# Optimization experiments

Measured on AMD Instinct MI355X. Metric: run time of the kernel, lower is better.

Reference implementation:

```python
import jax, jax.numpy as jnp
import numpy as np

IN_NC = 7


def setup_inputs() -> dict:
    key = jax.random.key(0)
    ks = jax.random.split(key, 32)
    B, H, W = 4, 192, 192
    Cf, O, L = 64, 64, 32  # in_fea, out_fea, len=max(64//16,32)
    d = {}
    d['fea'] = jax.random.normal(ks[0], (B, Cf, H, W), jnp.float32)
    d['inputs'] = jax.random.normal(ks[1], (B, IN_NC, H, W), jnp.float32)
    j = 2
    for i in range(3):
        k = 2 * i + 1
        oc = IN_NC * 3 * k * k
        d['dw_w%d' % i] = jax.random.normal(ks[j], (Cf, 1, k, k), jnp.float32) * 0.05; j += 1
        d['dw_b%d' % i] = jnp.zeros((Cf,), jnp.float32)
        d['pw_w%d' % i] = jax.random.normal(ks[j], (oc, Cf), jnp.float32) * 0.05; j += 1
        d['pw_b%d' % i] = jnp.zeros((oc,), jnp.float32)
        d['dcn_w%d' % i] = jax.random.normal(ks[j], (O, IN_NC, k, k), jnp.float32) * 0.05; j += 1
        d['dcn_b%d' % i] = jnp.zeros((O,), jnp.float32)
    d['attn_w'] = jax.random.normal(ks[j], (O, 3 * O), jnp.float32) * 0.05; j += 1
    d['attn_b'] = jnp.zeros((O,), jnp.float32)
    d['fc_w'] = jax.random.normal(ks[j], (L, O), jnp.float32) * 0.05; j += 1
    d['fc_b'] = jnp.zeros((L,), jnp.float32)
    for i in range(3):
        d['fcs_w%d' % i] = jax.random.normal(ks[j], (O, L), jnp.float32) * 0.05; j += 1
        d['fcs_b%d' % i] = jnp.zeros((O,), jnp.float32)
    d['conv_w'] = jax.random.normal(ks[j], (O, 3 * O), jnp.float32) * 0.05; j += 1
    d['conv_b'] = jnp.zeros((O,), jnp.float32)
    return d


def _dw_conv(x, w, b):
    # depthwise conv, stride 1, SAME padding (pad = k//2 for odd k)
    y = jax.lax.conv_general_dilated(x, w, window_strides=(1, 1), padding='SAME',
                                     dimension_numbers=('NCHW', 'OIHW', 'NCHW'),
                                     feature_group_count=x.shape[1])
    return y + b[None, :, None, None]


def _pw_conv(x, w, b):
    return jnp.einsum('bchw,oc->bohw', x, w) + b[None, :, None, None]


def _mdcn(x, offset, mask, w, b, k):
    # Modulated deformable conv, deformable_groups == C (one channel per group),
    # stride 1, padding k//2. offset: [B, C*2*K, H, W] as (c, k, (dy,dx)); mask: [B, C*K, H, W].
    B, C, H, W = x.shape
    K = k * k
    pad = k // 2
    off = offset.reshape(B, C, K, 2, H, W)
    m = mask.reshape(B, C, K, H, W)
    ky = (jnp.arange(K) // k).astype(jnp.float32)
    kx = (jnp.arange(K) % k).astype(jnp.float32)
    py = off[:, :, :, 0] + (ky[:, None, None] + jnp.arange(H, dtype=jnp.float32)[None, :, None] - pad)
    px = off[:, :, :, 1] + (kx[:, None, None] + jnp.arange(W, dtype=jnp.float32)[None, None, :] - pad)
    y0 = jnp.floor(py)
    x0 = jnp.floor(px)
    wy = py - y0
    wx = px - x0
    bi = jnp.arange(B)[:, None, None, None, None]
    ci = jnp.arange(C)[None, :, None, None, None]

    def gather(yi, xi):
        valid = (yi >= 0) & (yi < H) & (xi >= 0) & (xi < W)
        yc = jnp.clip(yi, 0, H - 1).astype(jnp.int32)
        xc = jnp.clip(xi, 0, W - 1).astype(jnp.int32)
        return jnp.where(valid, x[bi, ci, yc, xc], 0.0)

    v00 = gather(y0, x0)
    v01 = gather(y0, x0 + 1)
    v10 = gather(y0 + 1, x0)
    v11 = gather(y0 + 1, x0 + 1)
    samp = (v00 * (1 - wy) * (1 - wx) + v01 * (1 - wy) * wx
            + v10 * wy * (1 - wx) + v11 * wy * wx) * m  # [B,C,K,H,W]
    O = w.shape[0]
    return jnp.einsum('bckhw,ock->bohw', samp, w.reshape(O, C, K)) + b[None, :, None, None]


def reference(fea, inputs,
              dw_w0, dw_b0, pw_w0, pw_b0, dcn_w0, dcn_b0,
              dw_w1, dw_b1, pw_w1, pw_b1, dcn_w1, dcn_b1,
              dw_w2, dw_b2, pw_w2, pw_b2, dcn_w2, dcn_b2,
              attn_w, attn_b, fc_w, fc_b,
              fcs_w0, fcs_b0, fcs_w1, fcs_b1, fcs_w2, fcs_b2,
              conv_w, conv_b):
    dw_w = [dw_w0, dw_w1, dw_w2]; dw_b = [dw_b0, dw_b1, dw_b2]
    pw_w = [pw_w0, pw_w1, pw_w2]; pw_b = [pw_b0, pw_b1, pw_b2]
    dcn_w = [dcn_w0, dcn_w1, dcn_w2]; dcn_b = [dcn_b0, dcn_b1, dcn_b2]
    fcs_w = [fcs_w0, fcs_w1, fcs_w2]; fcs_b = [fcs_b0, fcs_b1, fcs_b2]
    outs = []
    for i in range(3):
        k = 2 * i + 1
        ds = k * k
        om = _pw_conv(_dw_conv(fea, dw_w[i], dw_b[i]), pw_w[i], pw_b[i])
        offset = om[:, :IN_NC * 2 * ds]
        mask = jax.nn.sigmoid(om[:, IN_NC * 2 * ds:])
        outs.append(jax.nn.relu(_mdcn(inputs, offset, mask, dcn_w[i], dcn_b[i], k)))
    out = jnp.stack(outs, axis=1)  # [B, 3, O, H, W]
    B, T, C, H, W = out.shape
    att = jax.nn.relu(_pw_conv(out.reshape(B, T * C, H, W), attn_w, attn_b))
    att = jnp.mean(att, axis=(2, 3), keepdims=True)  # GAP -> [B, O, 1, 1]
    att = jax.nn.relu(_pw_conv(att, fc_w, fc_b))      # [B, L, 1, 1]
    atts = jnp.stack([_pw_conv(att, fcs_w[i], fcs_b[i]) for i in range(3)], axis=1)  # [B,3,O,1,1]
    out = out * atts
    out = jax.nn.relu(_pw_conv(out.reshape(B, T * C, H, W), conv_w, conv_b))
    return out
```

## Files before the change

### kernel.cpp

```cpp
#include <hip/hip_runtime.h>
#include <math.h>

#define HH 192
#define WW 192
#define HWP (192*192)
#define BB 4
#define CF 64
#define NC 7
#define OO 64
#define NTOT (BB*HWP)
#define PIX_BLOCKS (HWP/256)

typedef float f32x16 __attribute__((ext_vector_type(16)));
typedef float f32x4  __attribute__((ext_vector_type(4)));

template<int k>
__global__ __launch_bounds__(256)
void dwv_kernel(const float* __restrict__ fea, const float* __restrict__ w,
                const float* __restrict__ bias, float* __restrict__ out) {
    constexpr int pad = k / 2;
    int idx = blockIdx.x * 256 + threadIdx.x;
    int xq = idx % 48;
    int x0 = xq * 4;
    int hpos = (idx / 48) % HH;
    int plane = idx / (48 * HH);
    int c = plane % CF;
    const float* f = fea + (size_t)plane * HWP;

    float wk[k * k];
#pragma unroll
    for (int i = 0; i < k * k; ++i) wk[i] = w[c * k * k + i];

    float acc0 = 0.f, acc1 = 0.f, acc2 = 0.f, acc3 = 0.f;
#pragma unroll
    for (int dy = 0; dy < k; ++dy) {
        int y = hpos + dy - pad;
        if (y < 0 || y >= HH) continue;
        const float* row = f + y * WW;
        float4 q0 = (x0 >= 4) ? *(const float4*)(row + x0 - 4) : make_float4(0.f, 0.f, 0.f, 0.f);
        float4 q1 = *(const float4*)(row + x0);
        float4 q2 = (x0 + 4 < WW) ? *(const float4*)(row + x0 + 4) : make_float4(0.f, 0.f, 0.f, 0.f);
        float wnd[8] = {q0.z, q0.w, q1.x, q1.y, q1.z, q1.w, q2.x, q2.y};
#pragma unroll
        for (int dx = 0; dx < k; ++dx) {
            float wt = wk[dy * k + dx];
            acc0 += wnd[0 + dx + 2 - pad] * wt;
            acc1 += wnd[1 + dx + 2 - pad] * wt;
            acc2 += wnd[2 + dx + 2 - pad] * wt;
            acc3 += wnd[3 + dx + 2 - pad] * wt;
        }
    }
    float b = bias[c];
    float4 o = make_float4(acc0 + b, acc1 + b, acc2 + b, acc3 + b);
    *(float4*)(out + (size_t)plane * HWP + hpos * WW + x0) = o;
}

__global__ void transpose_kernel(const float* __restrict__ in, float* __restrict__ out,
                                 int rows, int cols) {
    int idx = blockIdx.x * 256 + threadIdx.x;
    if (idx >= rows * cols) return;
    int r = idx / cols, c = idx % cols;
    out[c * rows + r] = in[idx];
}

__global__ __launch_bounds__(256)
void pw_gemm_kernel(const float* __restrict__ pw_w, const float* __restrict__ pw_b,
                    const float* __restrict__ dw, float* __restrict__ om,
                    int src0, int n_yx, int src1, int M) {
    __shared__ float As[64][68];
    __shared__ float Bs[64][132];
    const int ntiles = NTOT / 128;
    int ntile = blockIdx.x % ntiles;
    int mtile = blockIdx.x / ntiles;
    int nb0 = ntile * 128;
    int mb0 = mtile * 64;
    int tid = threadIdx.x;

    {
        int m = tid & 63;
        int kq = tid >> 6;
        int gm = mb0 + m;
        int srow = (gm < M) ? ((gm < n_yx) ? (src0 + gm) : (src1 + (gm - n_yx))) : src0;
        const float* ap = pw_w + (size_t)srow * CF;
#pragma unroll
        for (int i = 0; i < 4; ++i) {
            int k0 = (kq * 4 + i) * 4;
            float4 v = *(const float4*)(ap + k0);
            As[k0 + 0][m] = v.x; As[k0 + 1][m] = v.y;
            As[k0 + 2][m] = v.z; As[k0 + 3][m] = v.w;
        }
    }
    {
        int b = nb0 / HWP;
        int p0 = nb0 % HWP;
        const float* bp = dw + (size_t)b * CF * HWP + p0;
#pragma unroll
        for (int i = 0; i < 8; ++i) {
            int idx = tid + i * 256;
            int kk = idx >> 5;
            int f4 = idx & 31;
            float4 v = *(const float4*)(bp + (size_t)kk * HWP + f4 * 4);
            *(float4*)&Bs[kk][f4 * 4] = v;
        }
    }
    __syncthreads();

    int tm = (tid & 15) * 4;
    int tn = (tid >> 4) * 8;
    f32x4 aA0 = 0.f, aA1 = 0.f, aB0 = 0.f, aB1 = 0.f;
    f32x4 aC0 = 0.f, aC1 = 0.f, aD0 = 0.f, aD1 = 0.f;
#pragma unroll 8
    for (int kk = 0; kk < 64; ++kk) {
        f32x4 a  = *(const f32x4*)&As[kk][tm];
        f32x4 b0 = *(const f32x4*)&Bs[kk][tn];
        f32x4 b1 = *(const f32x4*)&Bs[kk][tn + 4];
#pragma unroll
        for (int j = 0; j < 4; ++j) {
            aA0[j] += a[0] * b0[j];  aA1[j] += a[0] * b1[j];
            aB0[j] += a[1] * b0[j];  aB1[j] += a[1] * b1[j];
            aC0[j] += a[2] * b0[j];  aC1[j] += a[2] * b1[j];
            aD0[j] += a[3] * b0[j];  aD1[j] += a[3] * b1[j];
        }
    }
    {
        int gm = mb0 + tm;
        float* dst = om + (size_t)gm * NTOT + nb0 + tn;
        if (gm < M) {
            float bi = pw_b[(gm < n_yx) ? (src0 + gm) : (src1 + gm - n_yx)];
#pragma unroll
            for (int j = 0; j < 4; ++j) { dst[j] = aA0[j] + bi; dst[4 + j] = aA1[j] + bi; }
        }
        gm++; dst += NTOT;
        if (gm < M) {
            float bi = pw_b[(gm < n_yx) ? (src0 + gm) : (src1 + gm - n_yx)];
#pragma unroll
            for (int j = 0; j < 4; ++j) { dst[j] = aB0[j] + bi; dst[4 + j] = aB1[j] + bi; }
        }
        gm++; dst += NTOT;
        if (gm < M) {
            float bi = pw_b[(gm < n_yx) ? (src0 + gm) : (src1 + gm - n_yx)];
#pragma unroll
            for (int j = 0; j < 4; ++j) { dst[j] = aC0[j] + bi; dst[4 + j] = aC1[j] + bi; }
        }
        gm++; dst += NTOT;
        if (gm < M) {
            float bi = pw_b[(gm < n_yx) ? (src0 + gm) : (src1 + gm - n_yx)];
#pragma unroll
            for (int j = 0; j < 4; ++j) { dst[j] = aD0[j] + bi; dst[4 + j] = aD1[j] + bi; }
        }
    }
}

template<int k>
__global__ __launch_bounds__(256)
void sample_kernel(const float* __restrict__ om, const float* __restrict__ inputs,
                   float* __restrict__ sbuf, int t0, int t1) {
    constexpr int K = k * k;
    constexpr int pad = k / 2;
    const int T = t1 - t0;
    int g = blockIdx.x / (NTOT / 256);
    int nb = blockIdx.x % (NTOT / 256);
    int n = nb * 256 + threadIdx.x;
    int b = n / HWP, p = n % HWP;
    int h = p / WW, wq = p % WW;
    const float* inb = inputs + (size_t)b * NC * HWP;
    int half = (T + 1) >> 1;
    int i0 = g * half;
    int i1 = min(T, i0 + half);
#pragma unroll 2
    for (int i = i0; i < i1; ++i) {
        int r = t0 + i;
        float oy = om[(size_t)(2 * i) * NTOT + n];
        float ox = om[(size_t)(2 * i + 1) * NTOT + n];
        float mr = om[(size_t)(2 * T + i) * NTOT + n];
        int c = r / K;
        int kk = r - c * K;
        int ky = kk / k, kx = kk - ky * k;
        const float* inc_ = inb + (size_t)c * HWP;
        float m = 1.f / (1.f + __expf(-mr));
        float py = oy + (float)(ky + h - pad);
        float px = ox + (float)(kx + wq - pad);
        float y0 = floorf(py), x0 = floorf(px);
        float wyf = py - y0, wxf = px - x0;
        int iy0 = (int)y0, ix0 = (int)x0;
        bool y0v = (iy0 >= 0) && (iy0 < HH);
        bool y1v = (iy0 + 1 >= 0) && (iy0 + 1 < HH);
        bool x0v = (ix0 >= 0) && (ix0 < WW);
        bool x1v = (ix0 + 1 >= 0) && (ix0 + 1 < WW);
        int yc0 = min(max(iy0, 0), HH - 1), yc1 = min(max(iy0 + 1, 0), HH - 1);
        int xc0 = min(max(ix0, 0), WW - 1), xc1 = min(max(ix0 + 1, 0), WW - 1);
        float v00 = 0.f, v01 = 0.f, v10 = 0.f, v11 = 0.f;
        if (y0v) {
            if (x0v) v00 = inc_[yc0 * WW + xc0];
            if (x1v) v01 = inc_[yc0 * WW + xc1];
        }
        if (y1v) {
            if (x0v) v10 = inc_[yc1 * WW + xc0];
            if (x1v) v11 = inc_[yc1 * WW + xc1];
        }
        float s = (v00 * (1.f - wyf) * (1.f - wxf) + v01 * (1.f - wyf) * wxf +
                   v10 * wyf * (1.f - wxf) + v11 * wyf * wxf) * m;
        sbuf[(size_t)i * NTOT + n] = s;
    }
}

__global__ __launch_bounds__(256)
void acc_gemm_kernel(const float* __restrict__ wt,
                     const float* __restrict__ bias,
                     const float* __restrict__ sbuf,
                     float* __restrict__ outbuf, int t_slot,
                     int t0, int t1, int flags) {
    __shared__ float As[64][68];
    __shared__ float Bs[64][132];
    const int T = t1 - t0;
    int nb0 = blockIdx.x * 128;
    int tid = threadIdx.x;

    for (int i4 = tid; i4 < T * 16; i4 += 256) {
        int row = i4 >> 4, c4 = (i4 & 15) * 4;
        float4 v = *(const float4*)(wt + (size_t)(t0 + row) * OO + c4);
        As[row][c4] = v.x; As[row][c4 + 1] = v.y; As[row][c4 + 2] = v.z; As[row][c4 + 3] = v.w;
    }
    for (int i4 = tid; i4 < T * 32; i4 += 256) {
        int row = i4 >> 5, f4 = (i4 & 31) * 4;
        float4 v = *(const float4*)(sbuf + (size_t)row * NTOT + nb0 + f4);
        *(float4*)&Bs[row][f4] = v;
    }
    __syncthreads();

    int tm = (tid & 15) * 4;
    int tn = (tid >> 4) * 8;
    f32x4 aA0 = 0.f, aA1 = 0.f, aB0 = 0.f, aB1 = 0.f;
    f32x4 aC0 = 0.f, aC1 = 0.f, aD0 = 0.f, aD1 = 0.f;
#pragma unroll 2
    for (int kk = 0; kk < T; ++kk) {
        f32x4 a  = *(const f32x4*)&As[kk][tm];
        f32x4 b0 = *(const f32x4*)&Bs[kk][tn];
        f32x4 b1 = *(const f32x4*)&Bs[kk][tn + 4];
#pragma unroll
        for (int j = 0; j < 4; ++j) {
            aA0[j] += a[0] * b0[j];  aA1[j] += a[0] * b1[j];
            aB0[j] += a[1] * b0[j];  aB1[j] += a[1] * b1[j];
            aC0[j] += a[2] * b0[j];  aC1[j] += a[2] * b1[j];
            aD0[j] += a[3] * b0[j];  aD1[j] += a[3] * b1[j];
        }
    }

    int b = nb0 / HWP, p0 = nb0 % HWP;
    f32x4 accs[8] = {aA0, aA1, aB0, aB1, aC0, aC1, aD0, aD1};
#pragma unroll
    for (int row = 0; row < 4; ++row) {
        int ch = tm + row;
        float* ptr = outbuf + ((size_t)((b * 3 + t_slot) * OO + ch)) * HWP + p0 + tn;
        f32x4 lo = accs[row * 2], hi = accs[row * 2 + 1];
        if (!(flags & 1)) {
            f32x4 o0 = *(const f32x4*)ptr;
            f32x4 o1 = *(const f32x4*)(ptr + 4);
#pragma unroll
            for (int j = 0; j < 4; ++j) { lo[j] += o0[j]; hi[j] += o1[j]; }
        }
        if (flags & 2) {
            float bi = bias[ch];
#pragma unroll
            for (int j = 0; j < 4; ++j) {
                lo[j] += bi; hi[j] += bi;
                lo[j] = lo[j] > 0.f ? lo[j] : 0.f;
                hi[j] = hi[j] > 0.f ? hi[j] : 0.f;
            }
        }
        *(f32x4*)ptr = lo;
        *(f32x4*)(ptr + 4) = hi;
    }
}

__global__ __launch_bounds__(256)
void branch_k1_kernel(const float* __restrict__ fea,
                      const float* __restrict__ dw_w0, const float* __restrict__ dw_b0,
                      const float* __restrict__ pw_w, const float* __restrict__ pw_b,
                      const float* __restrict__ inputs,
                      const float* __restrict__ dcn_wt, const float* __restrict__ dcn_b,
                      float* __restrict__ outbuf) {
    __shared__ float lw[21 * 64];
    for (int i = threadIdx.x; i < 21 * 16; i += 256)
        ((float4*)lw)[i] = ((const float4*)pw_w)[i];
    __syncthreads();
    int gid = blockIdx.x;
    int b = gid / PIX_BLOCKS;
    int p = (gid % PIX_BLOCKS) * 256 + threadIdx.x;
    int h = p / WW, wq = p % WW;
    const float* inb = inputs + (size_t)b * NC * HWP;

    f32x16 dwv0, dwv1, dwv2, dwv3;
    {
        const float* fp = fea + (size_t)(b * CF) * HWP + p;
#pragma unroll
        for (int j = 0; j < 16; ++j) dwv0[j] = fp[(size_t)j * HWP] * dw_w0[j] + dw_b0[j];
#pragma unroll
        for (int j = 0; j < 16; ++j) dwv1[j] = fp[(size_t)(16 + j) * HWP] * dw_w0[16 + j] + dw_b0[16 + j];
#pragma unroll
        for (int j = 0; j < 16; ++j) dwv2[j] = fp[(size_t)(32 + j) * HWP] * dw_w0[32 + j] + dw_b0[32 + j];
#pragma unroll
        for (int j = 0; j < 16; ++j) dwv3[j] = fp[(size_t)(48 + j) * HWP] * dw_w0[48 + j] + dw_b0[48 + j];
    }
    f32x16 acc0, acc1, acc2, acc3;
#pragma unroll
    for (int j = 0; j < 16; ++j) { acc0[j] = 0.f; acc1[j] = 0.f; acc2[j] = 0.f; acc3[j] = 0.f; }

    for (int r = 0; r < NC; ++r) {
        const float* wy = lw + (2 * r) * 64;
        const float* wx = wy + 64;
        const float* wm = lw + (14 + r) * 64;
        const float* inc_ = inb + (size_t)r * HWP;
        float oy = pw_b[2 * r], ox = pw_b[2 * r + 1], om = pw_b[14 + r];
#pragma unroll
        for (int j = 0; j < 16; ++j) { oy += wy[j] * dwv0[j];      ox += wx[j] * dwv0[j];      om += wm[j] * dwv0[j]; }
#pragma unroll
        for (int j = 0; j < 16; ++j) { oy += wy[16 + j] * dwv1[j]; ox += wx[16 + j] * dwv1[j]; om += wm[16 + j] * dwv1[j]; }
#pragma unroll
        for (int j = 0; j < 16; ++j) { oy += wy[32 + j] * dwv2[j]; ox += wx[32 + j] * dwv2[j]; om += wm[32 + j] * dwv2[j]; }
#pragma unroll
        for (int j = 0; j < 16; ++j) { oy += wy[48 + j] * dwv3[j]; ox += wx[48 + j] * dwv3[j]; om += wm[48 + j] * dwv3[j]; }
        float m = 1.f / (1.f + __expf(-om));
        float py = oy + (float)h;
        float px = ox + (float)wq;
        float y0 = floorf(py), x0 = floorf(px);
        float wyf = py - y0, wxf = px - x0;
        int iy0 = (int)y0, ix0 = (int)x0;
        bool y0v = (iy0 >= 0) && (iy0 < HH);
        bool y1v = (iy0 + 1 >= 0) && (iy0 + 1 < HH);
        bool x0v = (ix0 >= 0) && (ix0 < WW);
        bool x1v = (ix0 + 1 >= 0) && (ix0 + 1 < WW);
        int yc0 = min(max(iy0, 0), HH - 1), yc1 = min(max(iy0 + 1, 0), HH - 1);
        int xc0 = min(max(ix0, 0), WW - 1), xc1 = min(max(ix0 + 1, 0), WW - 1);
        float v00 = 0.f, v01 = 0.f, v10 = 0.f, v11 = 0.f;
        if (y0v) {
            if (x0v) v00 = inc_[yc0 * WW + xc0];
            if (x1v) v01 = inc_[yc0 * WW + xc1];
        }
        if (y1v) {
            if (x0v) v10 = inc_[yc1 * WW + xc0];
            if (x1v) v11 = inc_[yc1 * WW + xc1];
        }
        float s = (v00 * (1.f - wyf) * (1.f - wxf) + v01 * (1.f - wyf) * wxf +
                   v10 * wyf * (1.f - wxf) + v11 * wyf * wxf) * m;
        const float* dt = dcn_wt + (size_t)r * OO;
#pragma unroll
        for (int j = 0; j < 16; ++j) acc0[j] += s * dt[j];
#pragma unroll
        for (int j = 0; j < 16; ++j) acc1[j] += s * dt[16 + j];
#pragma unroll
        for (int j = 0; j < 16; ++j) acc2[j] += s * dt[32 + j];
#pragma unroll
        for (int j = 0; j < 16; ++j) acc3[j] += s * dt[48 + j];
    }
    float* op = outbuf + (size_t)(b * 3 * OO) * HWP + p;
#pragma unroll
    for (int j = 0; j < 16; ++j) { float v = acc0[j] + dcn_b[j];      op[(size_t)j * HWP] = v > 0.f ? v : 0.f; }
#pragma unroll
    for (int j = 0; j < 16; ++j) { float v = acc1[j] + dcn_b[16 + j]; op[(size_t)(16 + j) * HWP] = v > 0.f ? v : 0.f; }
#pragma unroll
    for (int j = 0; j < 16; ++j) { float v = acc2[j] + dcn_b[32 + j]; op[(size_t)(32 + j) * HWP] = v > 0.f ? v : 0.f; }
#pragma unroll
    for (int j = 0; j < 16; ++j) { float v = acc3[j] + dcn_b[48 + j]; op[(size_t)(48 + j) * HWP] = v > 0.f ? v : 0.f; }
}

__global__ __launch_bounds__(256)
void attn_sum_kernel(const float* __restrict__ outbuf, const float* __restrict__ attn_wt,
                     const float* __restrict__ attn_b, float* __restrict__ partial) {
    int g = blockIdx.x & 1;
    int blk = blockIdx.x >> 1;
    int b = blk / PIX_BLOCKS;
    int pb = blk % PIX_BLOCKS;
    int p = pb * 256 + threadIdx.x;
    const float* ob = outbuf + (size_t)(b * 192) * HWP + p;
    f32x16 a0, a1;
#pragma unroll
    for (int j = 0; j < 16; ++j) { a0[j] = attn_b[g * 32 + j]; a1[j] = attn_b[g * 32 + 16 + j]; }
    for (int c = 0; c < 192; ++c) {
        float v = ob[(size_t)c * HWP];
        const float* wt = attn_wt + c * OO + g * 32;
#pragma unroll
        for (int j = 0; j < 16; ++j) a0[j] += v * wt[j];
#pragma unroll
        for (int j = 0; j < 16; ++j) a1[j] += v * wt[16 + j];
    }
    __shared__ float red[4][32];
    int lane = threadIdx.x & 63, wv = threadIdx.x >> 6;
#pragma unroll
    for (int o = 0; o < 32; ++o) {
        float v = (o < 16) ? a0[o] : a1[o - 16];
        v = v > 0.f ? v : 0.f;
        v += __shfl_down(v, 32);
        v += __shfl_down(v, 16);
        v += __shfl_down(v, 8);
        v += __shfl_down(v, 4);
        v += __shfl_down(v, 2);
        v += __shfl_down(v, 1);
        if (lane == 0) red[wv][o] = v;
    }
    __syncthreads();
    if (threadIdx.x < 32) {
        int o = threadIdx.x;
        partial[((size_t)(b * PIX_BLOCKS + pb) * 2 + g) * 32 + o] =
            red[0][o] + red[1][o] + red[2][o] + red[3][o];
    }
}

__global__ void attn_finish_kernel(const float* __restrict__ partial,
                                   const float* __restrict__ fc_w, const float* __restrict__ fc_b,
                                   const float* __restrict__ fcs_w0, const float* __restrict__ fcs_b0,
                                   const float* __restrict__ fcs_w1, const float* __restrict__ fcs_b1,
                                   const float* __restrict__ fcs_w2, const float* __restrict__ fcs_b2,
                                   float* __restrict__ atts) {
    int b = blockIdx.x;
    __shared__ float attm[OO];
    __shared__ float fcv[32];
    int tid = threadIdx.x;
    if (tid < OO) {
        int g = tid >> 5, o = tid & 31;
        float s = 0.f;
        for (int blk = 0; blk < PIX_BLOCKS; ++blk)
            s += partial[((size_t)(b * PIX_BLOCKS + blk) * 2 + g) * 32 + o];
        attm[tid] = s / (float)HWP;
    }
    __syncthreads();
    if (tid < 32) {
        float s = fc_b[tid];
        for (int o = 0; o < OO; ++o) s += fc_w[tid * OO + o] * attm[o];
        fcv[tid] = s > 0.f ? s : 0.f;
    }
    __syncthreads();
    if (tid < OO) {
        {
            float s = fcs_b0[tid];
            for (int j = 0; j < 32; ++j) s += fcs_w0[tid * 32 + j] * fcv[j];
            atts[b * 192 + 0 * OO + tid] = s;
        }
        {
            float s = fcs_b1[tid];
            for (int j = 0; j < 32; ++j) s += fcs_w1[tid * 32 + j] * fcv[j];
            atts[b * 192 + 1 * OO + tid] = s;
        }
        {
            float s = fcs_b2[tid];
            for (int j = 0; j < 32; ++j) s += fcs_w2[tid * 32 + j] * fcv[j];
            atts[b * 192 + 2 * OO + tid] = s;
        }
    }
}

__global__ __launch_bounds__(256)
void final_kernel(const float* __restrict__ outbuf, const float* __restrict__ atts,
                  const float* __restrict__ conv_wt, const float* __restrict__ conv_b,
                  float* __restrict__ out) {
    int g = blockIdx.x & 1;
    int blk = blockIdx.x >> 1;
    int b = blk / PIX_BLOCKS;
    int p = (blk % PIX_BLOCKS) * 256 + threadIdx.x;
    const float* ob = outbuf + (size_t)(b * 192) * HWP + p;
    const float* at = atts + b * 192;
    f32x16 a0, a1;
#pragma unroll
    for (int j = 0; j < 16; ++j) { a0[j] = conv_b[g * 32 + j]; a1[j] = conv_b[g * 32 + 16 + j]; }
    for (int c = 0; c < 192; ++c) {
        float v = ob[(size_t)c * HWP] * at[c];
        const float* wt = conv_wt + c * OO + g * 32;
#pragma unroll
        for (int j = 0; j < 16; ++j) a0[j] += v * wt[j];
#pragma unroll
        for (int j = 0; j < 16; ++j) a1[j] += v * wt[16 + j];
    }
    float* op = out + ((size_t)(b * OO) + g * 32) * HWP + p;
#pragma unroll
    for (int j = 0; j < 16; ++j) op[(size_t)j * HWP] = a0[j] > 0.f ? a0[j] : 0.f;
#pragma unroll
    for (int j = 0; j < 16; ++j) op[(size_t)(16 + j) * HWP] = a1[j] > 0.f ? a1[j] : 0.f;
}

extern "C" void kernel_launch(void* const* d_in, const int* in_sizes, int n_in,
                              void* d_out, int out_size, void* d_ws, size_t ws_size,
                              hipStream_t stream) {
    const float* fea    = (const float*)d_in[0];
    const float* inputs = (const float*)d_in[1];
    const float* dw_w[3]  = {(const float*)d_in[2],  (const float*)d_in[8],  (const float*)d_in[14]};
    const float* dw_b[3]  = {(const float*)d_in[3],  (const float*)d_in[9],  (const float*)d_in[15]};
    const float* pw_w[3]  = {(const float*)d_in[4],  (const float*)d_in[10], (const float*)d_in[16]};
    const float* pw_b[3]  = {(const float*)d_in[5],  (const float*)d_in[11], (const float*)d_in[17]};
    const float* dcn_w[3] = {(const float*)d_in[6],  (const float*)d_in[12], (const float*)d_in[18]};
    const float* dcn_b[3] = {(const float*)d_in[7],  (const float*)d_in[13], (const float*)d_in[19]};
    const float* attn_w = (const float*)d_in[20];
    const float* attn_b = (const float*)d_in[21];
    const float* fc_w   = (const float*)d_in[22];
    const float* fc_b   = (const float*)d_in[23];
    const float* fcs_w[3] = {(const float*)d_in[24], (const float*)d_in[26], (const float*)d_in[28]};
    const float* fcs_b[3] = {(const float*)d_in[25], (const float*)d_in[27], (const float*)d_in[29]};
    const float* conv_w = (const float*)d_in[30];
    const float* conv_b = (const float*)d_in[31];
    float* out = (float*)d_out;

    const size_t F_OUTBUF = (size_t)BB * 3 * OO * HWP;
    const size_t F_SMALL  = 36864 + 768 + 512 + 4096 + 11264 + 12288 + 12288;
    float* W = (float*)d_ws;
    float* outbuf = W;            W += F_OUTBUF;
    size_t avail = (ws_size / 4 > F_OUTBUF + F_SMALL) ? (ws_size / 4 - F_OUTBUF - F_SMALL) : 0;
    int T = (int)(avail / (4 * (size_t)NTOT));
    if (T > 64) T = 64;
    if (T < 1) T = 1;
    float* om = W;                W += (size_t)3 * T * NTOT;
    float* sbuf = W;              W += (size_t)T * NTOT;
    float* partial = W;           W += 36864;
    float* atts = W;              W += 768;
    float* dcn_wt0 = W;           W += 512;
    float* dcn_wt1 = W;           W += 4096;
    float* dcn_wt2 = W;           W += 11264;
    float* attn_wt = W;           W += 12288;
    float* conv_wt = W;           W += 12288;
    float* dwscr = out;

    transpose_kernel<<<(192 * 64 + 255) / 256, 256, 0, stream>>>(attn_w, attn_wt, 64, 192);
    transpose_kernel<<<(192 * 64 + 255) / 256, 256, 0, stream>>>(conv_w, conv_wt, 64, 192);
    transpose_kernel<<<(7 * 64 + 255) / 256, 256, 0, stream>>>(dcn_w[0], dcn_wt0, 64, 7);
    transpose_kernel<<<(63 * 64 + 255) / 256, 256, 0, stream>>>(dcn_w[1], dcn_wt1, 64, 63);
    transpose_kernel<<<(175 * 64 + 255) / 256, 256, 0, stream>>>(dcn_w[2], dcn_wt2, 64, 175);

    const int dwv_grid = (BB * CF * HH * 48) / 256;
    const int pix_grid = BB * PIX_BLOCKS;
    const int samp_grid = 2 * (NTOT / 256);
    const int acc_grid = NTOT / 128;
    const int ntiles = NTOT / 128;

    dwv_kernel<5><<<dwv_grid, 256, 0, stream>>>(fea, dw_w[2], dw_b[2], dwscr);
    {
        const int TT = 175;
        for (int t0 = 0; t0 < TT; t0 += T) {
            int t1 = (t0 + T < TT) ? (t0 + T) : TT;
            int Tc = t1 - t0, M = 3 * Tc;
            int mt = (M + 63) / 64;
            pw_gemm_kernel<<<mt * ntiles, 256, 0, stream>>>(pw_w[2], pw_b[2], dwscr, om,
                                                            2 * t0, 2 * Tc, 2 * TT + t0, M);
            sample_kernel<5><<<samp_grid, 256, 0, stream>>>(om, inputs, sbuf, t0, t1);
            int flags = (t0 == 0 ? 1 : 0) | (t1 == TT ? 2 : 0);
            acc_gemm_kernel<<<acc_grid, 256, 0, stream>>>(dcn_wt2, dcn_b[2], sbuf, outbuf,
                                                          2, t0, t1, flags);
        }
    }
    dwv_kernel<3><<<dwv_grid, 256, 0, stream>>>(fea, dw_w[1], dw_b[1], dwscr);
    {
        const int TT = 63;
        for (int t0 = 0; t0 < TT; t0 += T) {
            int t1 = (t0 + T < TT) ? (t0 + T) : TT;
            int Tc = t1 - t0, M = 3 * Tc;
            int mt = (M + 63) / 64;
            pw_gemm_kernel<<<mt * ntiles, 256, 0, stream>>>(pw_w[1], pw_b[1], dwscr, om,
                                                            2 * t0, 2 * Tc, 2 * TT + t0, M);
            sample_kernel<3><<<samp_grid, 256, 0, stream>>>(om, inputs, sbuf, t0, t1);
            int flags = (t0 == 0 ? 1 : 0) | (t1 == TT ? 2 : 0);
            acc_gemm_kernel<<<acc_grid, 256, 0, stream>>>(dcn_wt1, dcn_b[1], sbuf, outbuf,
                                                          1, t0, t1, flags);
        }
    }
    branch_k1_kernel<<<pix_grid, 256, 0, stream>>>(fea, dw_w[0], dw_b[0], pw_w[0], pw_b[0],
                                                   inputs, dcn_wt0, dcn_b[0], outbuf);

    attn_sum_kernel<<<2 * pix_grid, 256, 0, stream>>>(outbuf, attn_wt, attn_b, partial);
    attn_finish_kernel<<<BB, 64, 0, stream>>>(partial, fc_w, fc_b,
                                              fcs_w[0], fcs_b[0], fcs_w[1], fcs_b[1],
                                              fcs_w[2], fcs_b[2], atts);
    final_kernel<<<2 * pix_grid, 256, 0, stream>>>(outbuf, atts, conv_wt, conv_b, out);
}
```

Baseline: 741.3 us.

## Rewrite attention and final 1x1 convs as LDS-tiled register-blocked GEMMs

Replaces the per-pixel attention-sum and final 1x1-conv kernels with shared-memory tiled GEMM kernels. Each block covers 64 output channels by 128 pixels and loads weight and activation tiles into LDS in 64-channel chunks. Each thread computes a 4x8 register tile. The attention kernel reduces ReLU outputs across pixel groups in LDS and writes 64-wide partial sums, so the partial buffer is doubled. The aim is to stop reading outbuf twice (once per output-channel half) and to cut the scalar weight loads in the inner loop, at the cost of more LDS use and barriers.

```diff
diff --git a/kernel.cpp b/kernel.cpp
--- a/kernel.cpp
+++ b/kernel.cpp
@@ -10,6 +10,7 @@
 #define OO 64
 #define NTOT (BB*HWP)
 #define PIX_BLOCKS (HWP/256)
+#define PBLK2 (HWP/128)
 
 typedef float f32x16 __attribute__((ext_vector_type(16)));
 typedef float f32x4  __attribute__((ext_vector_type(4)));
@@ -365,44 +366,73 @@
 }
 
 __global__ __launch_bounds__(256)
-void attn_sum_kernel(const float* __restrict__ outbuf, const float* __restrict__ attn_wt,
-                     const float* __restrict__ attn_b, float* __restrict__ partial) {
-    int g = blockIdx.x & 1;
-    int blk = blockIdx.x >> 1;
-    int b = blk / PIX_BLOCKS;
-    int pb = blk % PIX_BLOCKS;
-    int p = pb * 256 + threadIdx.x;
-    const float* ob = outbuf + (size_t)(b * 192) * HWP + p;
-    f32x16 a0, a1;
-#pragma unroll
-    for (int j = 0; j < 16; ++j) { a0[j] = attn_b[g * 32 + j]; a1[j] = attn_b[g * 32 + 16 + j]; }
-    for (int c = 0; c < 192; ++c) {
-        float v = ob[(size_t)c * HWP];
-        const float* wt = attn_wt + c * OO + g * 32;
-#pragma unroll
-        for (int j = 0; j < 16; ++j) a0[j] += v * wt[j];
-#pragma unroll
-        for (int j = 0; j < 16; ++j) a1[j] += v * wt[16 + j];
-    }
-    __shared__ float red[4][32];
-    int lane = threadIdx.x & 63, wv = threadIdx.x >> 6;
-#pragma unroll
-    for (int o = 0; o < 32; ++o) {
-        float v = (o < 16) ? a0[o] : a1[o - 16];
-        v = v > 0.f ? v : 0.f;
-        v += __shfl_down(v, 32);
-        v += __shfl_down(v, 16);
-        v += __shfl_down(v, 8);
-        v += __shfl_down(v, 4);
-        v += __shfl_down(v, 2);
-        v += __shfl_down(v, 1);
-        if (lane == 0) red[wv][o] = v;
-    }
+void attn_gemm_kernel(const float* __restrict__ outbuf, const float* __restrict__ attn_wt,
+                      const float* __restrict__ attn_b, float* __restrict__ partial) {
+    __shared__ float As[64][68];
+    __shared__ float Bs[64][132];
+    __shared__ float red[16][68];
+    int nb0 = blockIdx.x * 128;
+    int b = nb0 / HWP, p0 = nb0 % HWP;
+    int tid = threadIdx.x;
+    int tm = (tid & 15) * 4;
+    int tn = (tid >> 4) * 8;
+
+    f32x4 aA0 = 0.f, aA1 = 0.f, aB0 = 0.f, aB1 = 0.f;
+    f32x4 aC0 = 0.f, aC1 = 0.f, aD0 = 0.f, aD1 = 0.f;
+    for (int kc = 0; kc < 3; ++kc) {
+        for (int i4 = tid; i4 < 64 * 16; i4 += 256) {
+            int row = i4 >> 4, c4 = (i4 & 15) * 4;
+            float4 v = *(const float4*)(attn_wt + (size_t)(kc * 64 + row) * OO + c4);
+            As[row][c4] = v.x; As[row][c4 + 1] = v.y; As[row][c4 + 2] = v.z; As[row][c4 + 3] = v.w;
+        }
+        const float* bp = outbuf + ((size_t)(b * 192 + kc * 64)) * HWP + p0;
+        for (int i4 = tid; i4 < 64 * 32; i4 += 256) {
+            int row = i4 >> 5, f4 = (i4 & 31) * 4;
+            float4 v = *(const float4*)(bp + (size_t)row * HWP + f4);
+            *(float4*)&Bs[row][f4] = v;
+        }
+        __syncthreads();
+#pragma unroll 4
+        for (int kk = 0; kk < 64; ++kk) {
+            f32x4 a  = *(const f32x4*)&As[kk][tm];
+            f32x4 b0 = *(const f32x4*)&Bs[kk][tn];
+            f32x4 b1 = *(const f32x4*)&Bs[kk][tn + 4];
+#pragma unroll
+            for (int j = 0; j < 4; ++j) {
+                aA0[j] += a[0] * b0[j];  aA1[j] += a[0] * b1[j];
+                aB0[j] += a[1] * b0[j];  aB1[j] += a[1] * b1[j];
+                aC0[j] += a[2] * b0[j];  aC1[j] += a[2] * b1[j];
+                aD0[j] += a[3] * b0[j];  aD1[j] += a[3] * b1[j];
+            }
+        }
+        __syncthreads();
+    }
+    float bsum[4];
+    {
+        f32x4 accs[8] = {aA0, aA1, aB0, aB1, aC0, aC1, aD0, aD1};
+#pragma unroll
+        for (int row = 0; row < 4; ++row) {
+            float bi = attn_b[tm + row];
+            float s = 0.f;
+#pragma unroll
+            for (int j = 0; j < 4; ++j) {
+                float v0 = accs[row * 2][j] + bi;
+                float v1 = accs[row * 2 + 1][j] + bi;
+                s += (v0 > 0.f ? v0 : 0.f) + (v1 > 0.f ? v1 : 0.f);
+            }
+            bsum[row] = s;
+        }
+    }
+    int pg = tid >> 4;
+#pragma unroll
+    for (int row = 0; row < 4; ++row) red[pg][tm + row] = bsum[row];
     __syncthreads();
-    if (threadIdx.x < 32) {
-        int o = threadIdx.x;
-        partial[((size_t)(b * PIX_BLOCKS + pb) * 2 + g) * 32 + o] =
-            red[0][o] + red[1][o] + red[2][o] + red[3][o];
+    if (tid < 64) {
+        float s = 0.f;
+#pragma unroll
+        for (int g = 0; g < 16; ++g) s += red[g][tid];
+        int lb = p0 / 128;
+        partial[((size_t)(b * PBLK2 + lb)) * OO + tid] = s;
     }
 }
 
@@ -417,10 +447,9 @@
     __shared__ float fcv[32];
     int tid = threadIdx.x;
     if (tid < OO) {
-        int g = tid >> 5, o = tid & 31;
         float s = 0.f;
-        for (int blk = 0; blk < PIX_BLOCKS; ++blk)
-            s += partial[((size_t)(b * PIX_BLOCKS + blk) * 2 + g) * 32 + o];
+        for (int blk = 0; blk < PBLK2; ++blk)
+            s += partial[((size_t)(b * PBLK2 + blk)) * OO + tid];
         attm[tid] = s / (float)HWP;
     }
     __syncthreads();
@@ -450,31 +479,66 @@
 }
 
 __global__ __launch_bounds__(256)
-void final_kernel(const float* __restrict__ outbuf, const float* __restrict__ atts,
-                  const float* __restrict__ conv_wt, const float* __restrict__ conv_b,
-                  float* __restrict__ out) {
-    int g = blockIdx.x & 1;
-    int blk = blockIdx.x >> 1;
-    int b = blk / PIX_BLOCKS;
-    int p = (blk % PIX_BLOCKS) * 256 + threadIdx.x;
-    const float* ob = outbuf + (size_t)(b * 192) * HWP + p;
+void final_gemm_kernel(const float* __restrict__ outbuf, const float* __restrict__ atts,
+                       const float* __restrict__ conv_wt, const float* __restrict__ conv_b,
+                       float* __restrict__ out) {
+    __shared__ float As[64][68];
+    __shared__ float Bs[64][132];
+    int nb0 = blockIdx.x * 128;
+    int b = nb0 / HWP, p0 = nb0 % HWP;
+    int tid = threadIdx.x;
+    int tm = (tid & 15) * 4;
+    int tn = (tid >> 4) * 8;
     const float* at = atts + b * 192;
-    f32x16 a0, a1;
-#pragma unroll
-    for (int j = 0; j < 16; ++j) { a0[j] = conv_b[g * 32 + j]; a1[j] = conv_b[g * 32 + 16 + j]; }
-    for (int c = 0; c < 192; ++c) {
-        float v = ob[(size_t)c * HWP] * at[c];
-        const float* wt = conv_wt + c * OO + g * 32;
-#pragma unroll
-        for (int j = 0; j < 16; ++j) a0[j] += v * wt[j];
-#pragma unroll
-        for (int j = 0; j < 16; ++j) a1[j] += v * wt[16 + j];
-    }
-    float* op = out + ((size_t)(b * OO) + g * 32) * HWP + p;
-#pragma unroll
-    for (int j = 0; j < 16; ++j) op[(size_t)j * HWP] = a0[j] > 0.f ? a0[j] : 0.f;
-#pragma unroll
-    for (int j = 0; j < 16; ++j) op[(size_t)(16 + j) * HWP] = a1[j] > 0.f ? a1[j] : 0.f;
+
+    f32x4 aA0 = 0.f, aA1 = 0.f, aB0 = 0.f, aB1 = 0.f;
+    f32x4 aC0 = 0.f, aC1 = 0.f, aD0 = 0.f, aD1 = 0.f;
+    for (int kc = 0; kc < 3; ++kc) {
+        for (int i4 = tid; i4 < 64 * 16; i4 += 256) {
+            int row = i4 >> 4, c4 = (i4 & 15) * 4;
+            float4 v = *(const float4*)(conv_wt + (size_t)(kc * 64 + row) * OO + c4);
+            As[row][c4] = v.x; As[row][c4 + 1] = v.y; As[row][c4 + 2] = v.z; As[row][c4 + 3] = v.w;
+        }
+        const float* bp = outbuf + ((size_t)(b * 192 + kc * 64)) * HWP + p0;
+        for (int i4 = tid; i4 < 64 * 32; i4 += 256) {
+            int row = i4 >> 5, f4 = (i4 & 31) * 4;
+            float sc = at[kc * 64 + row];
+            float4 v = *(const float4*)(bp + (size_t)row * HWP + f4);
+            Bs[row][f4] = v.x * sc; Bs[row][f4 + 1] = v.y * sc;
+            Bs[row][f4 + 2] = v.z * sc; Bs[row][f4 + 3] = v.w * sc;
+        }
+        __syncthreads();
+#pragma unroll 4
+        for (int kk = 0; kk < 64; ++kk) {
+            f32x4 a  = *(const f32x4*)&As[kk][tm];
+            f32x4 b0 = *(const f32x4*)&Bs[kk][tn];
+            f32x4 b1 = *(const f32x4*)&Bs[kk][tn + 4];
+#pragma unroll
+            for (int j = 0; j < 4; ++j) {
+                aA0[j] += a[0] * b0[j];  aA1[j] += a[0] * b1[j];
+                aB0[j] += a[1] * b0[j];  aB1[j] += a[1] * b1[j];
+                aC0[j] += a[2] * b0[j];  aC1[j] += a[2] * b1[j];
+                aD0[j] += a[3] * b0[j];  aD1[j] += a[3] * b1[j];
+            }
+        }
+        __syncthreads();
+    }
+    f32x4 accs[8] = {aA0, aA1, aB0, aB1, aC0, aC1, aD0, aD1};
+#pragma unroll
+    for (int row = 0; row < 4; ++row) {
+        int ch = tm + row;
+        float bi = conv_b[ch];
+        float* ptr = out + ((size_t)(b * OO + ch)) * HWP + p0 + tn;
+        f32x4 lo = accs[row * 2], hi = accs[row * 2 + 1];
+#pragma unroll
+        for (int j = 0; j < 4; ++j) {
+            lo[j] += bi; hi[j] += bi;
+            lo[j] = lo[j] > 0.f ? lo[j] : 0.f;
+            hi[j] = hi[j] > 0.f ? hi[j] : 0.f;
+        }
+        *(f32x4*)ptr = lo;
+        *(f32x4*)(ptr + 4) = hi;
+    }
 }
 
 extern "C" void kernel_launch(void* const* d_in, const int* in_sizes, int n_in,
@@ -499,7 +563,7 @@
     float* out = (float*)d_out;
 
     const size_t F_OUTBUF = (size_t)BB * 3 * OO * HWP;
-    const size_t F_SMALL  = 36864 + 768 + 512 + 4096 + 11264 + 12288 + 12288;
+    const size_t F_SMALL  = 73728 + 768 + 512 + 4096 + 11264 + 12288 + 12288;
     float* W = (float*)d_ws;
     float* outbuf = W;            W += F_OUTBUF;
     size_t avail = (ws_size / 4 > F_OUTBUF + F_SMALL) ? (ws_size / 4 - F_OUTBUF - F_SMALL) : 0;
@@ -508,7 +572,7 @@
     if (T < 1) T = 1;
     float* om = W;                W += (size_t)3 * T * NTOT;
     float* sbuf = W;              W += (size_t)T * NTOT;
-    float* partial = W;           W += 36864;
+    float* partial = W;           W += 73728;
     float* atts = W;              W += 768;
     float* dcn_wt0 = W;           W += 512;
     float* dcn_wt1 = W;           W += 4096;
@@ -562,9 +626,9 @@
     branch_k1_kernel<<<pix_grid, 256, 0, stream>>>(fea, dw_w[0], dw_b[0], pw_w[0], pw_b[0],
                                                    inputs, dcn_wt0, dcn_b[0], outbuf);
 
-    attn_sum_kernel<<<2 * pix_grid, 256, 0, stream>>>(outbuf, attn_wt, attn_b, partial);
+    attn_gemm_kernel<<<NTOT / 128, 256, 0, stream>>>(outbuf, attn_wt, attn_b, partial);
     attn_finish_kernel<<<BB, 64, 0, stream>>>(partial, fc_w, fc_b,
                                               fcs_w[0], fcs_b[0], fcs_w[1], fcs_b[1],
                                               fcs_w[2], fcs_b[2], atts);
-    final_kernel<<<2 * pix_grid, 256, 0, stream>>>(outbuf, atts, conv_wt, conv_b, out);
-}
+    final_gemm_kernel<<<NTOT / 128, 256, 0, stream>>>(outbuf, atts, conv_wt, conv_b, out);
+}
```

Measured after the change: 750.5 us. Within noise of the previous version (+1.2%).
